# Kernel tuning notes

Measured on AMD Instinct MI355X. Metric: run time of the kernel, lower is better.

The kernel has to match this reference:

```python
import jax, jax.numpy as jnp
import numpy as np

T, B, D, H, HH, OUT = 512, 128, 256, 1024, 256, 128
EPS = 1e-3

def _ln(x, gamma, beta):
    # layer_norm over feature dim, eps=0.001, matching torch reciprocal(sqrt(var+eps))
    m = jnp.mean(x, -1, keepdims=True)
    xs = x - m
    v = jnp.mean(xs * xs, -1, keepdims=True)
    return gamma * xs * jax.lax.rsqrt(v + EPS) + beta

def _ln_all(h, base, units, gamma, beta):
    # normalize each of `base` gate blocks independently over `units`
    b = h.shape[0]
    hr = h.reshape(b, base, units)
    m = jnp.mean(hr, -1, keepdims=True)
    xs = hr - m
    v = jnp.mean(xs * xs, -1, keepdims=True)
    hn = (xs * jax.lax.rsqrt(v + EPS)).reshape(b, base * units)
    return gamma * hn + beta

def setup_inputs() -> dict:
    key = jax.random.key(0)
    ks = jax.random.split(key, 12)
    return {
        "x": jax.random.normal(ks[0], (T, B, D), jnp.float32),
        "Wx": jax.random.normal(ks[1], (4 * H, D), jnp.float32) * (1.0 / np.sqrt(D)),
        "Wh": jax.random.normal(ks[2], (4 * H, H), jnp.float32) * (1.0 / np.sqrt(H)),
        "bias": jax.random.normal(ks[3], (4 * H,), jnp.float32) * 0.1,
        "lna_gamma": jnp.ones((4 * H,), jnp.float32),
        "lna_beta": jnp.zeros((4 * H,), jnp.float32),
        "ln_gamma": jnp.ones((H,), jnp.float32),
        "ln_beta": jnp.zeros((H,), jnp.float32),
        "zb": jax.random.normal(ks[4], (4, HH, HH), jnp.float32) * 0.01,   # ib/jb/fb/ob _zb
        "zbeta": jax.random.normal(ks[5], (4, HH, H), jnp.float32) * 0.01, # ib/jb/fb/ob _beta
        "zw_w": jax.random.normal(ks[6], (8, HH, HH), jnp.float32) * 0.01, # ix,jx,fx,ox,ih,jh,fh,oh _zw_w
        "zw_b": jnp.ones((8, HH), jnp.float32),
        "alpha": jnp.full((8, HH, H), 0.1 / HH, jnp.float32) + jax.random.normal(ks[7], (8, HH, H), jnp.float32) * 1e-4,
        "hyp_Wx": jax.random.normal(ks[8], (4 * HH, D + H), jnp.float32) * (1.0 / np.sqrt(D + H)),
        "hyp_bx": jnp.zeros((4 * HH,), jnp.float32),
        "hyp_Wh": jax.random.normal(ks[9], (4 * HH, HH), jnp.float32) * (1.0 / np.sqrt(HH)),
        "hyp_bh": jnp.zeros((4 * HH,), jnp.float32),
        "hyp_lna_gamma": jnp.ones((4 * HH,), jnp.float32),
        "hyp_lna_beta": jnp.zeros((4 * HH,), jnp.float32),
        "hyp_ln_gamma": jnp.ones((HH,), jnp.float32),
        "hyp_ln_beta": jnp.zeros((HH,), jnp.float32),
        "fc_W": jax.random.normal(ks[10], (OUT, H), jnp.float32) * (1.0 / np.sqrt(H)),
        "fc_b": jnp.zeros((OUT,), jnp.float32),
    }

def reference(x, Wx, Wh, bias, lna_gamma, lna_beta, ln_gamma, ln_beta, zb, zbeta,
              zw_w, zw_b, alpha, hyp_Wx, hyp_bx, hyp_Wh, hyp_bh,
              hyp_lna_gamma, hyp_lna_beta, hyp_ln_gamma, hyp_ln_beta, fc_W, fc_b):
    b4 = bias.reshape(4, H)

    def step(carry, xt):
        h, c, hh, ch = carry  # main (B,H), hyper (B,HH)
        # ---- hypernetwork LSTM cell (layer-norm LSTM) ----
        g = jnp.concatenate([xt, h], 1) @ hyp_Wx.T + hyp_bx + hh @ hyp_Wh.T + hyp_bh
        g = _ln_all(g, 4, HH, hyp_lna_gamma, hyp_lna_beta)
        hi, hf, hg, ho = jnp.split(g, 4, 1)  # ingate, forgetgate, cellgate, outgate
        ch_n = jax.nn.sigmoid(hf) * ch + jax.nn.sigmoid(hi) * jnp.tanh(hg)
        hyp = jax.nn.sigmoid(ho) * jnp.tanh(_ln(ch_n, hyp_ln_gamma, hyp_ln_beta))
        # ---- hyper-modulation: per-gate scale vectors and bias adjustments ----
        z = jnp.einsum('bq,kqp->kbp', hyp, zw_w) + zw_b[:, None, :]   # (8,B,HH)
        sc = jnp.einsum('kbp,kph->kbh', z, alpha)                     # (8,B,H)
        bz = jnp.einsum('bq,kqp->kbp', hyp, zb)                       # (4,B,HH)
        badj = jnp.einsum('kbp,kph->kbh', bz, zbeta)                  # (4,B,H)
        # ---- main LSTM gates (order i, j, f, o) ----
        xg = (xt @ Wx.T).reshape(B, 4, H).transpose(1, 0, 2)          # (4,B,H)
        hg2 = (h @ Wh.T).reshape(B, 4, H).transpose(1, 0, 2)          # (4,B,H)
        gates = sc[:4] * xg + sc[4:] * hg2 + b4[:, None, :] + badj    # (4,B,H)
        gates = _ln_all(gates.transpose(1, 0, 2).reshape(B, 4 * H), 4, H, lna_gamma, lna_beta)
        i, j, f, o = jnp.split(gates, 4, 1)
        c_n = jax.nn.sigmoid(f) * c + jax.nn.sigmoid(i) * jnp.tanh(j)
        h_n = jax.nn.sigmoid(o) * jnp.tanh(_ln(c_n, ln_gamma, ln_beta))
        return (h_n, c_n, hyp, ch_n), None

    init = (jnp.zeros((B, H), x.dtype), jnp.zeros((B, H), x.dtype),
            jnp.zeros((B, HH), x.dtype), jnp.zeros((B, HH), x.dtype))
    (h_f, _, _, _), _ = jax.lax.scan(step, init, x)
    return h_f @ fc_W.T + fc_b  # (B, OUT)
```

## Files before the change

### kernel.cpp

```cpp
#include <hip/hip_runtime.h>
#include <hip/hip_cooperative_groups.h>
#include <math.h>

namespace cg = cooperative_groups;

#define T_STEPS 512
#define BATCH   128
#define DIN     256
#define HMAIN   1024
#define HHYP    256
#define OUTN    128
#define EPS     1e-3f

#define KSPLIT_NONE (1<<30)

typedef __attribute__((ext_vector_type(4))) float f32x4;
typedef __attribute__((ext_vector_type(8))) short s16x8;

__device__ __forceinline__ float sigm(float x){ return 1.f/(1.f + expf(-x)); }

__device__ __forceinline__ unsigned short f2bf(float f){
    union { float f; unsigned u; } x; x.f = f;
    unsigned r = x.u + 0x7FFFu + ((x.u >> 16) & 1u);
    return (unsigned short)(r >> 16);
}

#define BM 32
#define BN 64
#define KT 32
__device__ void gemm_dev(const float* __restrict__ A1, int lda1, int ksplit,
                         const float* __restrict__ A2, int lda2,
                         const float* __restrict__ Bp, int ldb, int b_nk,
                         const float* __restrict__ bias,
                         float* __restrict__ C, int ldc,
                         int K, int k0, int mtile, int ntile)
{
    __shared__ __align__(16) float As[KT][BM+4];
    __shared__ __align__(16) float Bs[KT][BN+4];
    const int tid = threadIdx.x;
    const int mt = tid >> 4, nt = tid & 15;
    const int m0g = mtile*BM, n0g = ntile*BN;
    float acc[4][4];
    #pragma unroll
    for (int i=0;i<4;++i) { acc[i][0]=0;acc[i][1]=0;acc[i][2]=0;acc[i][3]=0; }
    for (int kt = 0; kt < K; kt += KT) {
        __syncthreads();
        #pragma unroll
        for (int i=0;i<8;++i){
            int e = tid + i*128;
            int m = e >> 5, k = e & 31;
            int gk = k0 + kt + k, gm = m0g + m;
            float v = (gk < ksplit) ? A1[(size_t)gm*lda1 + gk]
                                    : A2[(size_t)gm*lda2 + (gk - ksplit)];
            As[k][m] = v;
        }
        if (b_nk) {
            #pragma unroll
            for (int i=0;i<16;++i){
                int e = tid + i*128;
                int n = e >> 5, k = e & 31;
                Bs[k][n] = Bp[(size_t)(n0g + n)*ldb + (k0 + kt + k)];
            }
        } else {
            #pragma unroll
            for (int i=0;i<16;++i){
                int e = tid + i*128;
                int k = e >> 6, n = e & 63;
                Bs[k][n] = Bp[(size_t)(k0 + kt + k)*ldb + (n0g + n)];
            }
        }
        __syncthreads();
        #pragma unroll
        for (int k=0;k<KT;++k){
            float4 av = *(const float4*)(&As[k][4*mt]);
            float4 bv = *(const float4*)(&Bs[k][4*nt]);
            acc[0][0]+=av.x*bv.x; acc[0][1]+=av.x*bv.y; acc[0][2]+=av.x*bv.z; acc[0][3]+=av.x*bv.w;
            acc[1][0]+=av.y*bv.x; acc[1][1]+=av.y*bv.y; acc[1][2]+=av.y*bv.z; acc[1][3]+=av.y*bv.w;
            acc[2][0]+=av.z*bv.x; acc[2][1]+=av.z*bv.y; acc[2][2]+=av.z*bv.z; acc[2][3]+=av.z*bv.w;
            acc[3][0]+=av.w*bv.x; acc[3][1]+=av.w*bv.y; acc[3][2]+=av.w*bv.z; acc[3][3]+=av.w*bv.w;
        }
    }
    #pragma unroll
    for (int i=0;i<4;++i){
        int gm = m0g + 4*mt + i;
        #pragma unroll
        for (int j=0;j<4;++j){
            int gn = n0g + 4*nt + j;
            float v = acc[i][j];
            if (bias) v += bias[gn];
            C[(size_t)gm*ldc + gn] = v;
        }
    }
}

#define ASTR 40
__device__ void gemm_mfma(const float* __restrict__ A1, int lda1, int ksplit,
                          const float* __restrict__ A2, int lda2,
                          const unsigned short* __restrict__ B, int ldb,
                          const float* __restrict__ bias,
                          float* __restrict__ C, int ldc,
                          int K, int k0, int mtile, int ntile)
{
    __shared__ __align__(16) unsigned short As[32*ASTR];
    __shared__ __align__(16) unsigned short Bs[128*ASTR];
    const int tid = threadIdx.x;
    const int lane = tid & 63, w = tid >> 6;
    const int wm = (w >> 1) * 16, wn = (w & 1) * 64;
    const int fr = lane & 15, koff = (lane >> 4) * 8;
    const int m0g = mtile*32, n0g = ntile*128;

    f32x4 acc[4];
    #pragma unroll
    for (int j=0;j<4;++j) acc[j] = (f32x4){0.f,0.f,0.f,0.f};

    const int arow = tid >> 3, akc = (tid & 7) * 4;
    for (int kt = 0; kt < K; kt += 32) {
        __syncthreads();
        {
            int gk = k0 + kt + akc;
            int gm = m0g + arow;
            const float* src = (gk < ksplit) ? (A1 + (size_t)gm*lda1 + gk)
                                             : (A2 + (size_t)gm*lda2 + (gk - ksplit));
            float4 v = *(const float4*)src;
            unsigned short* d = &As[arow*ASTR + akc];
            d[0] = f2bf(v.x); d[1] = f2bf(v.y); d[2] = f2bf(v.z); d[3] = f2bf(v.w);
        }
        #pragma unroll
        for (int i=0;i<4;++i){
            int e = tid + i*256;
            int n = e >> 3, kc = (e & 7) * 4;
            ushort4 bv = *(const ushort4*)(B + (size_t)(n0g + n)*ldb + (k0 + kt + kc));
            unsigned short* d = &Bs[n*ASTR + kc];
            d[0] = bv.x; d[1] = bv.y; d[2] = bv.z; d[3] = bv.w;
        }
        __syncthreads();
        s16x8 af = *(const s16x8*)&As[(wm + fr)*ASTR + koff];
        #pragma unroll
        for (int j=0;j<4;++j){
            s16x8 bf = *(const s16x8*)&Bs[(wn + j*16 + fr)*ASTR + koff];
            acc[j] = __builtin_amdgcn_mfma_f32_16x16x32_bf16(af, bf, acc[j], 0, 0, 0);
        }
    }
    #pragma unroll
    for (int j=0;j<4;++j){
        int gn = n0g + wn + j*16 + fr;
        float bb = bias ? bias[gn] : 0.f;
        #pragma unroll
        for (int r=0;r<4;++r){
            int gm = m0g + wm + (lane >> 4)*4 + r;
            C[(size_t)gm*ldc + gn] = acc[j][r] + bb;
        }
    }
}

#define WSTR 264
template<int NF, bool AF32>
__device__ __forceinline__ void gemm_ws(
    const void* __restrict__ Aptr, int lda,
    const unsigned short* wtile,
    const float* __restrict__ bias,
    float* __restrict__ Cout, int ldc,
    int lane, int w)
{
    const int fr = lane & 15, kq = lane >> 4;
    f32x4 acc[2][NF];
    #pragma unroll
    for (int mf=0; mf<2; ++mf)
        #pragma unroll
        for (int nf=0; nf<NF; ++nf) acc[mf][nf] = (f32x4){0.f,0.f,0.f,0.f};
    const int r0 = w*32 + fr;
    #pragma unroll
    for (int kt=0; kt<256; kt+=32) {
        const int k = kt + kq*8;
        s16x8 a[2];
        #pragma unroll
        for (int mf=0; mf<2; ++mf) {
            const int row = r0 + mf*16;
            if (AF32) {
                const float* s = (const float*)Aptr + (size_t)row*lda + k;
                float4 v0 = *(const float4*)s;
                float4 v1 = *(const float4*)(s+4);
                union { s16x8 v; unsigned short u[8]; } tc;
                tc.u[0]=f2bf(v0.x); tc.u[1]=f2bf(v0.y); tc.u[2]=f2bf(v0.z); tc.u[3]=f2bf(v0.w);
                tc.u[4]=f2bf(v1.x); tc.u[5]=f2bf(v1.y); tc.u[6]=f2bf(v1.z); tc.u[7]=f2bf(v1.w);
                a[mf] = tc.v;
            } else {
                a[mf] = *(const s16x8*)((const unsigned short*)Aptr + (size_t)row*lda + k);
            }
        }
        #pragma unroll
        for (int nf=0; nf<NF; ++nf) {
            s16x8 b = *(const s16x8*)&wtile[(nf*16+fr)*WSTR + k];
            acc[0][nf] = __builtin_amdgcn_mfma_f32_16x16x32_bf16(a[0], b, acc[0][nf], 0,0,0);
            acc[1][nf] = __builtin_amdgcn_mfma_f32_16x16x32_bf16(a[1], b, acc[1][nf], 0,0,0);
        }
    }
    #pragma unroll
    for (int nf=0; nf<NF; ++nf) {
        const int col = nf*16 + fr;
        const float bb = bias ? bias[col] : 0.f;
        #pragma unroll
        for (int mf=0; mf<2; ++mf) {
            const int row = w*32 + mf*16 + kq*4;
            #pragma unroll
            for (int r=0; r<4; ++r)
                Cout[(size_t)(row+r)*ldc + col] = acc[mf][nf][r] + bb;
        }
    }
}

__device__ __forceinline__ void load_wtile(const unsigned short* __restrict__ src,
                                           int ld, unsigned short* dst, int rows, int tid)
{
    const int chunks = rows * 32;
    for (int cidx = tid; cidx < chunks; cidx += 256) {
        const int r = cidx >> 5, k8 = (cidx & 31) << 3;
        *(uint4*)&dst[r*WSTR + k8] = *(const uint4*)&src[(size_t)r*ld + k8];
    }
}

__global__ __launch_bounds__(256) void k_prep_convert(
    const float* __restrict__ hyp_Wx, const float* __restrict__ hyp_Wh,
    const float* __restrict__ hyp_bx, const float* __restrict__ hyp_bh,
    const float* __restrict__ Wx, const float* __restrict__ Wh,
    unsigned short* __restrict__ wcat1bf, unsigned short* __restrict__ wxbf,
    unsigned short* __restrict__ whbf, float* __restrict__ bias1,
    float* __restrict__ act1f, float* __restrict__ c, float* __restrict__ ch,
    unsigned int* __restrict__ act1bf_zero)
{
    size_t i = (size_t)blockIdx.x*256 + threadIdx.x;
    if (i < 1572864u) {
        int n = (int)(i / 1536), k = (int)(i % 1536);
        float v = (k < 1280) ? hyp_Wx[(size_t)n*1280 + k] : hyp_Wh[(size_t)n*256 + (k-1280)];
        wcat1bf[i] = f2bf(v); return;
    }
    i -= 1572864u;
    if (i < 1048576u) { wxbf[i] = f2bf(Wx[i]); return; }
    i -= 1048576u;
    if (i < 4194304u) { whbf[i] = f2bf(Wh[i]); return; }
    i -= 4194304u;
    if (i < 1024u) { bias1[i] = hyp_bx[i] + hyp_bh[i]; return; }
    i -= 1024u;
    if (i < 163840u) { act1f[i] = 0.f; return; }
    i -= 163840u;
    if (i < 131072u) { c[i] = 0.f; return; }
    i -= 131072u;
    if (i < 32768u) { ch[i] = 0.f; return; }
    i -= 32768u;
    if (i < 81920u && act1bf_zero) { act1bf_zero[i] = 0u; return; }
}
#define PREP_TOTAL 7225568u

__global__ __launch_bounds__(128) void k_prep_wcomb(
    const float* __restrict__ zw_w, const float* __restrict__ zb,
    const float* __restrict__ alpha, const float* __restrict__ zbeta,
    float* __restrict__ wcombf32)
{
    int kk = blockIdx.z;
    const float* A = (kk < 8) ? (zw_w + (size_t)kk*65536) : (zb + (size_t)(kk-8)*65536);
    const float* Bm = (kk < 8) ? (alpha + (size_t)kk*262144) : (zbeta + (size_t)(kk-8)*262144);
    gemm_dev(A, 256, KSPLIT_NONE, A, 256, Bm, 1024, 0, nullptr,
             wcombf32 + (size_t)kk*262144, 1024, 256, 0, blockIdx.x, blockIdx.y);
}

__global__ __launch_bounds__(256) void k_prep_cvtcomb(
    const float* __restrict__ wcombf32, unsigned short* __restrict__ wcombbf)
{
    size_t i = (size_t)blockIdx.x*256 + threadIdx.x;
    if (i >= 3145728u) return;
    int kk = (int)(i / 262144u);
    int r  = (int)(i % 262144u);
    int n = r / 256, k = r % 256;
    wcombbf[i] = f2bf(wcombf32[(size_t)kk*262144 + (size_t)k*1024 + n]);
}

__global__ __launch_bounds__(256) void k_prep_bcomb(
    const float* __restrict__ zw_b, const float* __restrict__ alpha,
    float* __restrict__ bcomb)
{
    int k = blockIdx.x;
    int n = blockIdx.y*256 + threadIdx.x;
    float s = 0.f;
    for (int p=0;p<256;++p)
        s += zw_b[k*256+p] * alpha[(size_t)k*262144 + (size_t)p*1024 + n];
    bcomb[(size_t)k*1024 + n] = s;
}

__device__ __forceinline__ void breduce2(float& a, float& b, volatile float* buf, int tid){
    #pragma unroll
    for (int off = 32; off > 0; off >>= 1) { a += __shfl_xor(a, off); b += __shfl_xor(b, off); }
    __syncthreads();
    if ((tid & 63) == 0) { buf[(tid>>6)*2] = a; buf[(tid>>6)*2+1] = b; }
    __syncthreads();
    a = buf[0] + buf[2] + buf[4] + buf[6];
    b = buf[1] + buf[3] + buf[5] + buf[7];
}

__device__ __forceinline__ void hyper_cell6(
    int b, int tid, volatile float* cbuf,
    const float* __restrict__ gpart, const float* __restrict__ bias1,
    const float* __restrict__ lna_g, const float* __restrict__ lna_b,
    const float* __restrict__ ln_g, const float* __restrict__ ln_b,
    float* __restrict__ ch, unsigned short* __restrict__ act1bf)
{
    float v[4];
    #pragma unroll
    for (int g=0; g<4; ++g){
        size_t idx = (size_t)b*1024 + g*256 + tid;
        v[g] = gpart[idx] + gpart[131072+idx] + gpart[262144+idx]
             + gpart[393216+idx] + gpart[524288+idx] + gpart[655360+idx]
             + bias1[g*256 + tid];
    }
    #pragma unroll
    for (int g=0; g<4; ++g){
        float s = v[g], ss = v[g]*v[g];
        breduce2(s, ss, cbuf, tid);
        float m = s * (1.f/256.f);
        float var = ss * (1.f/256.f) - m*m;
        v[g] = (v[g]-m)*rsqrtf(var + EPS)*lna_g[g*256+tid] + lna_b[g*256+tid];
    }
    float chp = ch[b*256 + tid];
    float cn = sigm(v[1])*chp + sigm(v[0])*tanhf(v[2]);
    float s = cn, ss = cn*cn;
    breduce2(s, ss, cbuf, tid);
    float m = s*(1.f/256.f);
    float var = ss*(1.f/256.f) - m*m;
    float hn = sigm(v[3]) * tanhf((cn-m)*rsqrtf(var + EPS)*ln_g[tid] + ln_b[tid]);
    ch[b*256 + tid] = cn;
    act1bf[(size_t)b*1280 + 1024 + tid] = f2bf(hn);
}

__device__ __forceinline__ void main_cell2(
    int b, int tid, volatile float* cbuf,
    const float* __restrict__ bias4,
    const float* __restrict__ lna_g, const float* __restrict__ lna_b,
    const float* __restrict__ ln_g, const float* __restrict__ ln_b,
    const float* __restrict__ xgbuf, const float* __restrict__ hgpart,
    const float* __restrict__ scb,
    float* __restrict__ c, unsigned short* __restrict__ act1bf,
    float* __restrict__ hfc)
{
    float gn[4][4];
    #pragma unroll
    for (int k=0;k<4;++k){
        float pre[4]; float s=0.f, ss=0.f;
        #pragma unroll
        for (int j=0;j<4;++j){
            int h = j*256 + tid;
            int n = k*1024 + h;
            size_t bh = (size_t)b*1024 + h;
            size_t bn = (size_t)b*4096 + n;
            float xgv = xgbuf[bn];
            float hgv = hgpart[bn] + hgpart[524288+bn] + hgpart[1048576+bn] + hgpart[1572864+bn];
            float p = scb[(size_t)k*131072 + bh]*xgv + scb[(size_t)(4+k)*131072 + bh]*hgv
                    + bias4[n] + scb[(size_t)(8+k)*131072 + bh];
            pre[j] = p; s += p; ss += p*p;
        }
        breduce2(s, ss, cbuf, tid);
        float m = s*(1.f/1024.f);
        float var = ss*(1.f/1024.f) - m*m;
        float rs = rsqrtf(var + EPS);
        #pragma unroll
        for (int j=0;j<4;++j){
            int h=j*256+tid, n=k*1024+h;
            gn[k][j] = (pre[j]-m)*rs*lna_g[n] + lna_b[n];
        }
    }
    float cnv[4]; float s=0.f, ss=0.f;
    #pragma unroll
    for (int j=0;j<4;++j){
        int h=j*256+tid;
        float cv = c[(size_t)b*1024+h];
        float x = sigm(gn[2][j])*cv + sigm(gn[0][j])*tanhf(gn[1][j]);
        cnv[j]=x; s+=x; ss+=x*x;
    }
    breduce2(s, ss, cbuf, tid);
    float m=s*(1.f/1024.f);
    float var=ss*(1.f/1024.f)-m*m;
    float rs=rsqrtf(var + EPS);
    #pragma unroll
    for (int j=0;j<4;++j){
        int h=j*256+tid;
        float hv = sigm(gn[3][j])*tanhf((cnv[j]-m)*rs*ln_g[h] + ln_b[h]);
        c[(size_t)b*1024+h] = cnv[j];
        act1bf[(size_t)b*1280 + h] = f2bf(hv);
        hfc[(size_t)b*1024 + h] = hv;
    }
}

__device__ __forceinline__ void hyper_cell_body(
    const float* __restrict__ lna_g, const float* __restrict__ lna_b,
    const float* __restrict__ ln_g, const float* __restrict__ ln_b,
    const float* __restrict__ gpart, const float* __restrict__ bias1,
    float* __restrict__ ch, float* __restrict__ act1, int b, int tid)
{
    __shared__ float buf[8];
    float v[4];
    #pragma unroll
    for (int g=0; g<4; ++g){
        int idx = b*1024 + g*256 + tid;
        v[g] = gpart[idx] + gpart[131072 + idx] + gpart[262144 + idx] + gpart[393216 + idx]
             + bias1[g*256 + tid];
    }
    #pragma unroll
    for (int g=0; g<4; ++g){
        float s = v[g], ss = v[g]*v[g];
        breduce2(s, ss, buf, tid);
        float m = s * (1.f/256.f);
        float var = ss * (1.f/256.f) - m*m;
        v[g] = (v[g]-m)*rsqrtf(var + EPS)*lna_g[g*256+tid] + lna_b[g*256+tid];
    }
    float chp = ch[b*256 + tid];
    float cn = sigm(v[1])*chp + sigm(v[0])*tanhf(v[2]);
    float s = cn, ss = cn*cn;
    breduce2(s, ss, buf, tid);
    float m = s*(1.f/256.f);
    float var = ss*(1.f/256.f) - m*m;
    float hn = sigm(v[3]) * tanhf((cn-m)*rsqrtf(var + EPS)*ln_g[tid] + ln_b[tid]);
    ch[b*256 + tid] = cn;
    act1[b*1280 + 1024 + tid] = hn;
}

__device__ __forceinline__ void main_cell_body(
    const float* __restrict__ bias4,
    const float* __restrict__ lna_g, const float* __restrict__ lna_b,
    const float* __restrict__ ln_g, const float* __restrict__ ln_b,
    const float* __restrict__ xghg, const float* __restrict__ scb,
    float* __restrict__ c, float* __restrict__ act1, int b, int tid)
{
    __shared__ float buf[8];
    float gn[4][4];
    #pragma unroll
    for (int k=0;k<4;++k){
        float pre[4]; float s=0.f, ss=0.f;
        #pragma unroll
        for (int j=0;j<4;++j){
            int h = j*256 + tid;
            int n = k*1024 + h;
            int bh = b*1024 + h;
            float xgv = xghg[b*4096 + n];
            float hgv = xghg[524288 + b*4096 + n];
            float p = scb[k*131072 + bh]*xgv + scb[(4+k)*131072 + bh]*hgv
                    + bias4[n] + scb[(8+k)*131072 + bh];
            pre[j] = p; s += p; ss += p*p;
        }
        breduce2(s, ss, buf, tid);
        float m = s*(1.f/1024.f);
        float var = ss*(1.f/1024.f) - m*m;
        float rs = rsqrtf(var + EPS);
        #pragma unroll
        for (int j=0;j<4;++j){
            int h=j*256+tid, n=k*1024+h;
            gn[k][j] = (pre[j]-m)*rs*lna_g[n] + lna_b[n];
        }
    }
    float cnv[4]; float s=0.f, ss=0.f;
    #pragma unroll
    for (int j=0;j<4;++j){
        int h=j*256+tid;
        float cv = c[b*1024+h];
        float x = sigm(gn[2][j])*cv + sigm(gn[0][j])*tanhf(gn[1][j]);
        cnv[j]=x; s+=x; ss+=x*x;
    }
    breduce2(s, ss, buf, tid);
    float m=s*(1.f/1024.f);
    float var=ss*(1.f/1024.f)-m*m;
    float rs=rsqrtf(var + EPS);
    #pragma unroll
    for (int j=0;j<4;++j){
        int h=j*256+tid;
        float hv = sigm(gn[3][j])*tanhf((cnv[j]-m)*rs*ln_g[h] + ln_b[h]);
        c[b*1024+h] = cnv[j];
        act1[b*1280 + h] = hv;
    }
}

__global__ __launch_bounds__(256) void k_step1(
    const float* __restrict__ xt, const float* __restrict__ act1,
    const unsigned short* __restrict__ wcat1bf,
    const unsigned short* __restrict__ wxbf, const unsigned short* __restrict__ whbf,
    float* __restrict__ gpart, float* __restrict__ xghg)
{
    int bid = blockIdx.x;
    if (bid < 128) {
        int sp = bid >> 5, r = bid & 31;
        gemm_mfma(xt, 256, 256, act1, 1280, wcat1bf, 1536, nullptr,
                  gpart + (size_t)sp*131072, 1024, 384, sp*384, r >> 3, r & 7);
    } else if (bid < 256) {
        int r = bid - 128;
        gemm_mfma(xt, 256, KSPLIT_NONE, xt, 256, wxbf, 256, nullptr,
                  xghg, 4096, 256, 0, r >> 5, r & 31);
    } else {
        int r = bid - 256;
        gemm_mfma(act1, 1280, KSPLIT_NONE, act1, 1280, whbf, 1024, nullptr,
                  xghg + 524288, 4096, 1024, 0, r >> 5, r & 31);
    }
}

__global__ __launch_bounds__(256) void k_step2(
    const float* __restrict__ act1, const unsigned short* __restrict__ wcombbf,
    const float* __restrict__ bcomb, float* __restrict__ scb)
{
    int bid = blockIdx.x;
    int kk = bid >> 5, r = bid & 31;
    const float* bias = (kk < 8) ? (bcomb + (size_t)kk*1024) : nullptr;
    gemm_mfma(act1 + 1024, 1280, KSPLIT_NONE, act1 + 1024, 1280,
              wcombbf + (size_t)kk*262144, 256, bias,
              scb + (size_t)kk*131072, 1024, 256, 0, r >> 3, r & 7);
}

__global__ __launch_bounds__(256) void k_hyper_cell(
    const float* __restrict__ lna_g, const float* __restrict__ lna_b,
    const float* __restrict__ ln_g, const float* __restrict__ ln_b,
    const float* __restrict__ gpart, const float* __restrict__ bias1,
    float* __restrict__ ch, float* __restrict__ act1)
{
    hyper_cell_body(lna_g, lna_b, ln_g, ln_b, gpart, bias1, ch, act1,
                    blockIdx.x, threadIdx.x);
}

__global__ __launch_bounds__(256) void k_main_cell(
    const float* __restrict__ bias4,
    const float* __restrict__ lna_g, const float* __restrict__ lna_b,
    const float* __restrict__ ln_g, const float* __restrict__ ln_b,
    const float* __restrict__ xghg, const float* __restrict__ scb,
    float* __restrict__ c, float* __restrict__ act1)
{
    main_cell_body(bias4, lna_g, lna_b, ln_g, ln_b, xghg, scb, c, act1,
                   blockIdx.x, threadIdx.x);
}

__global__ __launch_bounds__(256, 2) void k_persist2(
    const float* __restrict__ x,
    const unsigned short* __restrict__ wcat1bf,
    const unsigned short* __restrict__ wxbf,
    const unsigned short* __restrict__ whbf,
    const unsigned short* __restrict__ wcombbf,
    const float* __restrict__ bcomb, const float* __restrict__ bias1,
    const float* __restrict__ bias4,
    const float* __restrict__ lna_g, const float* __restrict__ lna_b,
    const float* __restrict__ ln_g, const float* __restrict__ ln_b,
    const float* __restrict__ hlna_g, const float* __restrict__ hlna_b,
    const float* __restrict__ hln_g, const float* __restrict__ hln_b,
    float* __restrict__ gpart, float* __restrict__ hgpart,
    float* __restrict__ xgbuf, float* __restrict__ scb,
    unsigned short* __restrict__ act1bf, float* __restrict__ hfc,
    float* __restrict__ c, float* __restrict__ ch)
{
    cg::grid_group grid = cg::this_grid();
    const int bid = blockIdx.x, tid = threadIdx.x;
    const int lane = tid & 63, w = tid >> 6;
    __shared__ __align__(16) unsigned short wlds[25344];
    __shared__ float cbuf[8];

    if (bid < 96) {
        load_wtile(wcat1bf + (size_t)((bid & 15)*64)*1536 + (bid >> 4)*256,
                   1536, wlds, 64, tid);
    } else if (bid < 352) {
        int h_ = bid - 96;
        load_wtile(whbf + (size_t)((h_ >> 2)*64)*1024 + (h_ & 3)*256,
                   1024, wlds, 64, tid);
    } else if (bid < 416) {
        load_wtile(wxbf + (size_t)(bid - 352)*64*256, 256, wlds, 64, tid);
    }
    if (bid < 384) {
        int kk = bid >> 5, mt = bid & 31;
        load_wtile(wcombbf + (size_t)kk*262144 + (size_t)(mt*32)*256,
                   256, wlds + 16896, 32, tid);
    }
    __syncthreads();

    for (int t = 0; t < T_STEPS; ++t) {
        const float* xt = x + (size_t)t*BATCH*DIN;

        if (bid < 96) {
            int nt = bid & 15, sp = bid >> 4;
            float* outp = gpart + (size_t)sp*131072 + nt*64;
            if (sp == 0)
                gemm_ws<4,true >(xt, 256, wlds, nullptr, outp, 1024, lane, w);
            else
                gemm_ws<4,false>(act1bf + (sp-1)*256, 1280, wlds, nullptr, outp, 1024, lane, w);
        }
        grid.sync();

        if (bid >= 96 && bid < 352) {
            int h_ = bid - 96, nt = h_ >> 2, sp = h_ & 3;
            gemm_ws<4,false>(act1bf + sp*256, 1280, wlds, nullptr,
                             hgpart + (size_t)sp*524288 + nt*64, 4096, lane, w);
        } else if (bid >= 352 && bid < 416) {
            gemm_ws<4,true >(xt, 256, wlds, nullptr,
                             xgbuf + (bid - 352)*64, 4096, lane, w);
        } else {
            int row = (bid >= 416) ? (bid - 416) : (bid < 32 ? 96 + bid : -1);
            if (row >= 0)
                hyper_cell6(row, tid, cbuf, gpart, bias1,
                            hlna_g, hlna_b, hln_g, hln_b, ch, act1bf);
        }
        grid.sync();

        if (bid < 384) {
            int kk = bid >> 5, mt = bid & 31;
            const float* bp = (kk < 8) ? (bcomb + (size_t)kk*1024 + mt*32) : nullptr;
            gemm_ws<2,false>(act1bf + 1024, 1280, wlds + 16896, bp,
                             scb + (size_t)kk*131072 + mt*32, 1024, lane, w);
        }
        grid.sync();

        if (bid < 128)
            main_cell2(bid, tid, cbuf, bias4, lna_g, lna_b, ln_g, ln_b,
                       xgbuf, hgpart, scb, c, act1bf, hfc);
        grid.sync();
    }
}

__global__ __launch_bounds__(128) void k_fc2(
    const float* __restrict__ fcW, const float* __restrict__ fcb,
    const float* __restrict__ hsrc, int ldh, float* __restrict__ out)
{
    int b = blockIdx.x, o = threadIdx.x;
    const float* h = hsrc + (size_t)b*ldh;
    float s = fcb[o];
    for (int k=0;k<1024;++k) s += h[k]*fcW[(size_t)o*1024 + k];
    out[b*OUTN + o] = s;
}

extern "C" void kernel_launch(void* const* d_in, const int* in_sizes, int n_in,
                              void* d_out, int out_size, void* d_ws, size_t ws_size,
                              hipStream_t stream)
{
    const float* x        = (const float*)d_in[0];
    const float* Wx       = (const float*)d_in[1];
    const float* Wh       = (const float*)d_in[2];
    const float* bias     = (const float*)d_in[3];
    const float* lna_g    = (const float*)d_in[4];
    const float* lna_b    = (const float*)d_in[5];
    const float* ln_g     = (const float*)d_in[6];
    const float* ln_b     = (const float*)d_in[7];
    const float* zb       = (const float*)d_in[8];
    const float* zbeta    = (const float*)d_in[9];
    const float* zw_w     = (const float*)d_in[10];
    const float* zw_b     = (const float*)d_in[11];
    const float* alpha    = (const float*)d_in[12];
    const float* hyp_Wx   = (const float*)d_in[13];
    const float* hyp_bx   = (const float*)d_in[14];
    const float* hyp_Wh   = (const float*)d_in[15];
    const float* hyp_bh   = (const float*)d_in[16];
    const float* hlna_g   = (const float*)d_in[17];
    const float* hlna_b   = (const float*)d_in[18];
    const float* hln_g    = (const float*)d_in[19];
    const float* hln_b    = (const float*)d_in[20];
    const float* fcW      = (const float*)d_in[21];
    const float* fcb      = (const float*)d_in[22];
    float* out = (float*)d_out;

    unsigned short* wcat1bf = (unsigned short*)d_ws;
    unsigned short* wxbf    = wcat1bf + 1572864;
    unsigned short* whbf    = wxbf + 1048576;
    unsigned short* wcombbf = whbf + 4194304;
    unsigned short* act1bf  = wcombbf + 3145728;
    float* fbase = (float*)(act1bf + 163840);
    float* bcomb = fbase;
    float* bias1 = bcomb + 8192;
    float* hfc   = bias1 + 1024;
    float* c     = hfc + 131072;
    float* ch    = c + 131072;
    float* act1o = ch + 32768;
    float* gpart = act1o + 163840;
    float* hgpart= gpart + 786432;
    float* xgbuf = hgpart + 2097152;
    float* scb   = xgbuf + 524288;
    float* wcombf32 = gpart;

    k_prep_convert<<<(PREP_TOTAL + 255)/256, 256, 0, stream>>>(
        hyp_Wx, hyp_Wh, hyp_bx, hyp_bh, Wx, Wh,
        wcat1bf, wxbf, whbf, bias1, act1o, c, ch, (unsigned int*)act1bf);
    k_prep_wcomb<<<dim3(8,16,12), 128, 0, stream>>>(zw_w, zb, alpha, zbeta, wcombf32);
    k_prep_bcomb<<<dim3(8,4), 256, 0, stream>>>(zw_b, alpha, bcomb);
    k_prep_cvtcomb<<<(3145728 + 255)/256, 256, 0, stream>>>(wcombf32, wcombbf);

    static int use_coop = -1;
    if (use_coop < 0) {
        use_coop = 0;
        int dev = 0;
        if (hipGetDevice(&dev) == hipSuccess) {
            hipDeviceProp_t prop;
            if (hipGetDeviceProperties(&prop, dev) == hipSuccess &&
                prop.cooperativeLaunch) {
                int occ = 0;
                if (hipOccupancyMaxActiveBlocksPerMultiprocessor(
                        &occ, (const void*)k_persist2, 256, 0) == hipSuccess &&
                    occ >= 2 && occ * prop.multiProcessorCount >= 512) {
                    use_coop = 1;
                }
            }
        }
    }

    int coop_launched = 0;
    if (use_coop) {
        void* cargs[] = {
            (void*)&x, (void*)&wcat1bf, (void*)&wxbf, (void*)&whbf, (void*)&wcombbf,
            (void*)&bcomb, (void*)&bias1, (void*)&bias,
            (void*)&lna_g, (void*)&lna_b, (void*)&ln_g, (void*)&ln_b,
            (void*)&hlna_g, (void*)&hlna_b, (void*)&hln_g, (void*)&hln_b,
            (void*)&gpart, (void*)&hgpart, (void*)&xgbuf, (void*)&scb,
            (void*)&act1bf, (void*)&hfc, (void*)&c, (void*)&ch
        };
        hipError_t e = hipLaunchCooperativeKernel((const void*)k_persist2,
                                                  dim3(512), dim3(256),
                                                  cargs, 0u, stream);
        if (e == hipSuccess) {
            coop_launched = 1;
        } else {
            (void)hipGetLastError();
            use_coop = 0;
        }
    }

    if (!coop_launched) {
        float* xghg = hgpart;
        for (int t = 0; t < T_STEPS; ++t) {
            const float* xt = x + (size_t)t*BATCH*DIN;
            k_step1<<<384, 256, 0, stream>>>(xt, act1o, wcat1bf, wxbf, whbf, gpart, xghg);
            k_hyper_cell<<<BATCH, 256, 0, stream>>>(hlna_g, hlna_b, hln_g, hln_b,
                                                    gpart, bias1, ch, act1o);
            k_step2<<<384, 256, 0, stream>>>(act1o, wcombbf, bcomb, scb);
            k_main_cell<<<BATCH, 256, 0, stream>>>(bias, lna_g, lna_b, ln_g, ln_b,
                                                   xghg, scb, c, act1o);
        }
        k_fc2<<<BATCH, 128, 0, stream>>>(fcW, fcb, act1o, 1280, out);
        return;
    }

    k_fc2<<<BATCH, 128, 0, stream>>>(fcW, fcb, hfc, 1024, out);
}
```

Measured before the change: 34.20 ms.

## Replace cooperative grid.sync with relaxed-atomic sharded counter barrier

Swaps cooperative-groups grid.sync for a custom barrier that uses 16 padded counters, each advanced by a subset of blocks, with relaxed agent-scope atomics and sleep polling. Cross-block data is read and written with relaxed agent-scope atomic loads and stores instead of relying on the fences grid.sync provides. bf16 activation stores are packed in pairs into 32-bit atomic stores. The aim is to cut the per-step synchronization cost across 2048 barriers, but there is no acquire/release ordering, so memory visibility between steps is not guaranteed and races are possible.

```diff
diff --git a/kernel.cpp b/kernel.cpp
--- a/kernel.cpp
+++ b/kernel.cpp
@@ -1,8 +1,5 @@
 #include <hip/hip_runtime.h>
-#include <hip/hip_cooperative_groups.h>
 #include <math.h>
-
-namespace cg = cooperative_groups;
 
 #define T_STEPS 512
 #define BATCH   128
@@ -13,6 +10,7 @@
 #define EPS     1e-3f
 
 #define KSPLIT_NONE (1<<30)
+#define NBLK 512
 
 typedef __attribute__((ext_vector_type(4))) float f32x4;
 typedef __attribute__((ext_vector_type(8))) short s16x8;
@@ -23,6 +21,32 @@
     union { float f; unsigned u; } x; x.f = f;
     unsigned r = x.u + 0x7FFFu + ((x.u >> 16) & 1u);
     return (unsigned short)(r >> 16);
+}
+
+__device__ __forceinline__ float agf(const float* p){
+    return __hip_atomic_load(const_cast<float*>(p), __ATOMIC_RELAXED, __HIP_MEMORY_SCOPE_AGENT);
+}
+__device__ __forceinline__ unsigned long long agu8(const void* p){
+    return __hip_atomic_load(const_cast<unsigned long long*>((const unsigned long long*)p),
+                             __ATOMIC_RELAXED, __HIP_MEMORY_SCOPE_AGENT);
+}
+__device__ __forceinline__ void agsf(float* p, float v){
+    __hip_atomic_store(p, v, __ATOMIC_RELAXED, __HIP_MEMORY_SCOPE_AGENT);
+}
+__device__ __forceinline__ void agsu(unsigned* p, unsigned v){
+    __hip_atomic_store(p, v, __ATOMIC_RELAXED, __HIP_MEMORY_SCOPE_AGENT);
+}
+
+__device__ __forceinline__ void gbar(unsigned* cnt, unsigned phase, int bid, int tid){
+    __syncthreads();
+    if (tid < 16){
+        if (tid == (bid & 15))
+            __hip_atomic_fetch_add(&cnt[tid*32], 1u, __ATOMIC_RELAXED, __HIP_MEMORY_SCOPE_AGENT);
+        const unsigned tg = phase * (NBLK/16);
+        while (__hip_atomic_load(&cnt[tid*32], __ATOMIC_RELAXED, __HIP_MEMORY_SCOPE_AGENT) < tg)
+            __builtin_amdgcn_s_sleep(4);
+    }
+    __syncthreads();
 }
 
 #define BM 32
@@ -154,7 +178,7 @@
 }
 
 #define WSTR 264
-template<int NF, bool AF32>
+template<int NF, int AMODE>
 __device__ __forceinline__ void gemm_ws(
     const void* __restrict__ Aptr, int lda,
     const unsigned short* wtile,
@@ -176,7 +200,7 @@
         #pragma unroll
         for (int mf=0; mf<2; ++mf) {
             const int row = r0 + mf*16;
-            if (AF32) {
+            if (AMODE == 0) {
                 const float* s = (const float*)Aptr + (size_t)row*lda + k;
                 float4 v0 = *(const float4*)s;
                 float4 v1 = *(const float4*)(s+4);
@@ -185,7 +209,11 @@
                 tc.u[4]=f2bf(v1.x); tc.u[5]=f2bf(v1.y); tc.u[6]=f2bf(v1.z); tc.u[7]=f2bf(v1.w);
                 a[mf] = tc.v;
             } else {
-                a[mf] = *(const s16x8*)((const unsigned short*)Aptr + (size_t)row*lda + k);
+                const unsigned short* s = (const unsigned short*)Aptr + (size_t)row*lda + k;
+                union { unsigned long long q[2]; s16x8 v; } tc;
+                tc.q[0] = agu8(s);
+                tc.q[1] = agu8(s + 4);
+                a[mf] = tc.v;
             }
         }
         #pragma unroll
@@ -204,7 +232,7 @@
             const int row = w*32 + mf*16 + kq*4;
             #pragma unroll
             for (int r=0; r<4; ++r)
-                Cout[(size_t)(row+r)*ldc + col] = acc[mf][nf][r] + bb;
+                agsf(&Cout[(size_t)(row+r)*ldc + col], acc[mf][nf][r] + bb);
         }
     }
 }
@@ -226,7 +254,7 @@
     unsigned short* __restrict__ wcat1bf, unsigned short* __restrict__ wxbf,
     unsigned short* __restrict__ whbf, float* __restrict__ bias1,
     float* __restrict__ act1f, float* __restrict__ c, float* __restrict__ ch,
-    unsigned int* __restrict__ act1bf_zero)
+    unsigned int* __restrict__ act1bf_zero, unsigned int* __restrict__ gcnt_zero)
 {
     size_t i = (size_t)blockIdx.x*256 + threadIdx.x;
     if (i < 1572864u) {
@@ -247,9 +275,11 @@
     i -= 131072u;
     if (i < 32768u) { ch[i] = 0.f; return; }
     i -= 32768u;
-    if (i < 81920u && act1bf_zero) { act1bf_zero[i] = 0u; return; }
-}
-#define PREP_TOTAL 7225568u
+    if (i < 81920u) { act1bf_zero[i] = 0u; return; }
+    i -= 81920u;
+    if (i < 512u) { gcnt_zero[i] = 0u; return; }
+}
+#define PREP_TOTAL 7226880u
 
 __global__ __launch_bounds__(128) void k_prep_wcomb(
     const float* __restrict__ zw_w, const float* __restrict__ zb,
@@ -307,8 +337,8 @@
     #pragma unroll
     for (int g=0; g<4; ++g){
         size_t idx = (size_t)b*1024 + g*256 + tid;
-        v[g] = gpart[idx] + gpart[131072+idx] + gpart[262144+idx]
-             + gpart[393216+idx] + gpart[524288+idx] + gpart[655360+idx]
+        v[g] = agf(&gpart[idx]) + agf(&gpart[131072+idx]) + agf(&gpart[262144+idx])
+             + agf(&gpart[393216+idx]) + agf(&gpart[524288+idx]) + agf(&gpart[655360+idx])
              + bias1[g*256 + tid];
     }
     #pragma unroll
@@ -327,7 +357,10 @@
     float var = ss*(1.f/256.f) - m*m;
     float hn = sigm(v[3]) * tanhf((cn-m)*rsqrtf(var + EPS)*ln_g[tid] + ln_b[tid]);
     ch[b*256 + tid] = cn;
-    act1bf[(size_t)b*1280 + 1024 + tid] = f2bf(hn);
+    unsigned hb = f2bf(hn);
+    unsigned other = __shfl_down(hb, 1);
+    if (!(tid & 1))
+        agsu((unsigned*)(act1bf + (size_t)b*1280 + 1024 + tid), hb | (other << 16));
 }
 
 __device__ __forceinline__ void main_cell2(
@@ -350,10 +383,12 @@
             int n = k*1024 + h;
             size_t bh = (size_t)b*1024 + h;
             size_t bn = (size_t)b*4096 + n;
-            float xgv = xgbuf[bn];
-            float hgv = hgpart[bn] + hgpart[524288+bn] + hgpart[1048576+bn] + hgpart[1572864+bn];
-            float p = scb[(size_t)k*131072 + bh]*xgv + scb[(size_t)(4+k)*131072 + bh]*hgv
-                    + bias4[n] + scb[(size_t)(8+k)*131072 + bh];
+            float xgv = agf(&xgbuf[bn]);
+            float hgv = agf(&hgpart[bn]) + agf(&hgpart[524288+bn])
+                      + agf(&hgpart[1048576+bn]) + agf(&hgpart[1572864+bn]);
+            float p = agf(&scb[(size_t)k*131072 + bh])*xgv
+                    + agf(&scb[(size_t)(4+k)*131072 + bh])*hgv
+                    + bias4[n] + agf(&scb[(size_t)(8+k)*131072 + bh]);
             pre[j] = p; s += p; ss += p*p;
         }
         breduce2(s, ss, cbuf, tid);
@@ -383,8 +418,11 @@
         int h=j*256+tid;
         float hv = sigm(gn[3][j])*tanhf((cnv[j]-m)*rs*ln_g[h] + ln_b[h]);
         c[(size_t)b*1024+h] = cnv[j];
-        act1bf[(size_t)b*1280 + h] = f2bf(hv);
         hfc[(size_t)b*1024 + h] = hv;
+        unsigned hb = f2bf(hv);
+        unsigned other = __shfl_down(hb, 1);
+        if (!(tid & 1))
+            agsu((unsigned*)(act1bf + (size_t)b*1280 + h), hb | (other << 16));
     }
 }
 
@@ -530,7 +568,7 @@
                    blockIdx.x, threadIdx.x);
 }
 
-__global__ __launch_bounds__(256, 2) void k_persist2(
+__global__ __launch_bounds__(256, 2) void k_persist3(
     const float* __restrict__ x,
     const unsigned short* __restrict__ wcat1bf,
     const unsigned short* __restrict__ wxbf,
@@ -545,9 +583,9 @@
     float* __restrict__ gpart, float* __restrict__ hgpart,
     float* __restrict__ xgbuf, float* __restrict__ scb,
     unsigned short* __restrict__ act1bf, float* __restrict__ hfc,
-    float* __restrict__ c, float* __restrict__ ch)
-{
-    cg::grid_group grid = cg::this_grid();
+    float* __restrict__ c, float* __restrict__ ch,
+    unsigned* __restrict__ gcnt)
+{
     const int bid = blockIdx.x, tid = threadIdx.x;
     const int lane = tid & 63, w = tid >> 6;
     __shared__ __align__(16) unsigned short wlds[25344];
@@ -570,6 +608,7 @@
     }
     __syncthreads();
 
+    unsigned phase = 0;
     for (int t = 0; t < T_STEPS; ++t) {
         const float* xt = x + (size_t)t*BATCH*DIN;
 
@@ -577,39 +616,39 @@
             int nt = bid & 15, sp = bid >> 4;
             float* outp = gpart + (size_t)sp*131072 + nt*64;
             if (sp == 0)
-                gemm_ws<4,true >(xt, 256, wlds, nullptr, outp, 1024, lane, w);
+                gemm_ws<4,0>(xt, 256, wlds, nullptr, outp, 1024, lane, w);
             else
-                gemm_ws<4,false>(act1bf + (sp-1)*256, 1280, wlds, nullptr, outp, 1024, lane, w);
-        }
-        grid.sync();
+                gemm_ws<4,2>(act1bf + (sp-1)*256, 1280, wlds, nullptr, outp, 1024, lane, w);
+        }
+        gbar(gcnt, ++phase, bid, tid);
 
         if (bid >= 96 && bid < 352) {
             int h_ = bid - 96, nt = h_ >> 2, sp = h_ & 3;
-            gemm_ws<4,false>(act1bf + sp*256, 1280, wlds, nullptr,
-                             hgpart + (size_t)sp*524288 + nt*64, 4096, lane, w);
+            gemm_ws<4,2>(act1bf + sp*256, 1280, wlds, nullptr,
+                         hgpart + (size_t)sp*524288 + nt*64, 4096, lane, w);
         } else if (bid >= 352 && bid < 416) {
-            gemm_ws<4,true >(xt, 256, wlds, nullptr,
-                             xgbuf + (bid - 352)*64, 4096, lane, w);
+            gemm_ws<4,0>(xt, 256, wlds, nullptr,
+                         xgbuf + (bid - 352)*64, 4096, lane, w);
         } else {
             int row = (bid >= 416) ? (bid - 416) : (bid < 32 ? 96 + bid : -1);
             if (row >= 0)
                 hyper_cell6(row, tid, cbuf, gpart, bias1,
                             hlna_g, hlna_b, hln_g, hln_b, ch, act1bf);
         }
-        grid.sync();
+        gbar(gcnt, ++phase, bid, tid);
 
         if (bid < 384) {
             int kk = bid >> 5, mt = bid & 31;
             const float* bp = (kk < 8) ? (bcomb + (size_t)kk*1024 + mt*32) : nullptr;
-            gemm_ws<2,false>(act1bf + 1024, 1280, wlds + 16896, bp,
-                             scb + (size_t)kk*131072 + mt*32, 1024, lane, w);
-        }
-        grid.sync();
+            gemm_ws<2,2>(act1bf + 1024, 1280, wlds + 16896, bp,
+                         scb + (size_t)kk*131072 + mt*32, 1024, lane, w);
+        }
+        gbar(gcnt, ++phase, bid, tid);
 
         if (bid < 128)
             main_cell2(bid, tid, cbuf, bias4, lna_g, lna_b, ln_g, ln_b,
                        xgbuf, hgpart, scb, c, act1bf, hfc);
-        grid.sync();
+        gbar(gcnt, ++phase, bid, tid);
     }
 }
 
@@ -669,11 +708,13 @@
     float* hgpart= gpart + 786432;
     float* xgbuf = hgpart + 2097152;
     float* scb   = xgbuf + 524288;
+    unsigned* gcnt = (unsigned*)(scb + 1572864);
     float* wcombf32 = gpart;
 
     k_prep_convert<<<(PREP_TOTAL + 255)/256, 256, 0, stream>>>(
         hyp_Wx, hyp_Wh, hyp_bx, hyp_bh, Wx, Wh,
-        wcat1bf, wxbf, whbf, bias1, act1o, c, ch, (unsigned int*)act1bf);
+        wcat1bf, wxbf, whbf, bias1, act1o, c, ch,
+        (unsigned int*)act1bf, gcnt);
     k_prep_wcomb<<<dim3(8,16,12), 128, 0, stream>>>(zw_w, zb, alpha, zbeta, wcombf32);
     k_prep_bcomb<<<dim3(8,4), 256, 0, stream>>>(zw_b, alpha, bcomb);
     k_prep_cvtcomb<<<(3145728 + 255)/256, 256, 0, stream>>>(wcombf32, wcombbf);
@@ -688,8 +729,8 @@
                 prop.cooperativeLaunch) {
                 int occ = 0;
                 if (hipOccupancyMaxActiveBlocksPerMultiprocessor(
-                        &occ, (const void*)k_persist2, 256, 0) == hipSuccess &&
-                    occ >= 2 && occ * prop.multiProcessorCount >= 512) {
+                        &occ, (const void*)k_persist3, 256, 0) == hipSuccess &&
+                    occ >= 2 && occ * prop.multiProcessorCount >= NBLK) {
                     use_coop = 1;
                 }
             }
@@ -704,10 +745,10 @@
             (void*)&lna_g, (void*)&lna_b, (void*)&ln_g, (void*)&ln_b,
             (void*)&hlna_g, (void*)&hlna_b, (void*)&hln_g, (void*)&hln_b,
             (void*)&gpart, (void*)&hgpart, (void*)&xgbuf, (void*)&scb,
-            (void*)&act1bf, (void*)&hfc, (void*)&c, (void*)&ch
+            (void*)&act1bf, (void*)&hfc, (void*)&c, (void*)&ch, (void*)&gcnt
         };
-        hipError_t e = hipLaunchCooperativeKernel((const void*)k_persist2,
-                                                  dim3(512), dim3(256),
+        hipError_t e = hipLaunchCooperativeKernel((const void*)k_persist3,
+                                                  dim3(NBLK), dim3(256),
                                                   cargs, 0u, stream);
         if (e == hipSuccess) {
             coop_launched = 1;
```

After: 34.18 ms. About the same (-0.0%).
